# Kernel optimization log

Hardware: AMD Instinct MI355X
Metric: run time of the kernel (lower is better)

Reference implementation:

```python
import jax, jax.numpy as jnp
import numpy as np

EMBED_DIM = 1024
HEAD_DIM = 64


def setup_inputs() -> dict:
    key = jax.random.key(0)
    ks = jax.random.split(key, 7)
    s_in = EMBED_DIM ** -0.5  # torch Linear default init scale
    x = jax.random.normal(ks[0], (4, 4096, EMBED_DIM), dtype=jnp.float32)
    Wk = jax.random.uniform(ks[1], (HEAD_DIM, EMBED_DIM), jnp.float32, -s_in, s_in)
    bk = jax.random.uniform(ks[2], (HEAD_DIM,), jnp.float32, -s_in, s_in)
    Wq = jax.random.uniform(ks[3], (HEAD_DIM, EMBED_DIM), jnp.float32, -s_in, s_in)
    bq = jax.random.uniform(ks[4], (HEAD_DIM,), jnp.float32, -s_in, s_in)
    Wv = jax.random.uniform(ks[5], (HEAD_DIM, EMBED_DIM), jnp.float32, -s_in, s_in)
    bv = jax.random.uniform(ks[6], (HEAD_DIM,), jnp.float32, -s_in, s_in)
    return {"x": x, "Wq": Wq, "bq": bq, "Wk": Wk, "bk": bk, "Wv": Wv, "bv": bv}


def reference(x, Wq, bq, Wk, bk, Wv, bv):
    # torch Linear: y = x @ W.T + b
    q = jnp.einsum('btc,dc->btd', x, Wq) + bq  # [B,T,D]
    k = jnp.einsum('btc,dc->btd', x, Wk) + bk
    v = jnp.einsum('btc,dc->btd', x, Wv) + bv
    scale = HEAD_DIM ** -0.5
    # NOTE: original divides by scale (multiplies by sqrt(head_dim)) -- faithful
    scores = jnp.einsum('btd,bsd->bts', q, k) / scale  # [B,T,T]
    attn_weights = jax.nn.softmax(scores, axis=-1)
    return jnp.einsum('bts,bsd->btd', attn_weights, v)
```

## Files before the change

### kernel.cpp

```cpp
#include <hip/hip_runtime.h>

#define BATCH 4
#define SEQ   4096
#define CDIM  1024
#define DDIM  64
#define NROW  (BATCH * SEQ)
#define NSPL  8
#define SEG   (NROW * DDIM)

typedef _Float16 f16;
typedef _Float16 f16x8 __attribute__((ext_vector_type(8)));
typedef _Float16 f16x4 __attribute__((ext_vector_type(4)));
typedef __fp16   h16x2 __attribute__((ext_vector_type(2)));
typedef float    f32x4 __attribute__((ext_vector_type(4)));

#define MFMA32(a, b, c) __builtin_amdgcn_mfma_f32_16x16x32_f16((a), (b), (c), 0, 0, 0)
#define MFMA16(a, b, c) __builtin_amdgcn_mfma_f32_16x16x16f16((a), (b), (c), 0, 0, 0)

#define GLDS(g, l)                                                            \
  __builtin_amdgcn_global_load_lds((const __attribute__((address_space(1))) void*)(g), \
                                   (__attribute__((address_space(3))) void*)(l), 16, 0, 0)

#define QSCALE 11.5415603f

__device__ inline f16x8 cvt8(f32x4 a, f32x4 b) {
  h16x2 p0 = __builtin_amdgcn_cvt_pkrtz(a[0], a[1]);
  h16x2 p1 = __builtin_amdgcn_cvt_pkrtz(a[2], a[3]);
  h16x2 p2 = __builtin_amdgcn_cvt_pkrtz(b[0], b[1]);
  h16x2 p3 = __builtin_amdgcn_cvt_pkrtz(b[2], b[3]);
  f16x8 r;
  r[0] = p0[0]; r[1] = p0[1]; r[2] = p1[0]; r[3] = p1[1];
  r[4] = p2[0]; r[5] = p2[1]; r[6] = p3[0]; r[7] = p3[1];
  return r;
}

__device__ inline f16x4 cvt4(float a, float b, float c, float d) {
  h16x2 lo = __builtin_amdgcn_cvt_pkrtz(a, b);
  h16x2 hi = __builtin_amdgcn_cvt_pkrtz(c, d);
  f16x4 r;
  r[0] = lo[0]; r[1] = lo[1]; r[2] = hi[0]; r[3] = hi[1];
  return r;
}

__global__ __launch_bounds__(256) void prep_w_kernel(const float* __restrict__ Wq,
                                                     const float* __restrict__ Wk,
                                                     const float* __restrict__ Wv,
                                                     f16* __restrict__ wf2) {
  const int t = blockIdx.x * 256 + threadIdx.x;
  const int lane = t & 63;
  const int s = t >> 6;
  const int mt = s % 12, ck = s / 12;
  const int mat = mt >> 2, tile = mt & 3;
  const int n = lane & 15, quad = lane >> 4;
  const float* W = (mat == 0) ? Wq : (mat == 1) ? Wk : Wv;
  const float* src = W + (size_t)(tile * 16 + n) * CDIM + ck * 32 + quad * 8;
  const f32x4 a = *(const f32x4*)src;
  const f32x4 b = *(const f32x4*)(src + 4);
  *(f16x8*)(wf2 + (size_t)t * 8) = cvt8(a, b);
}

__global__ __launch_bounds__(512, 4) void proj_kernel(const float* __restrict__ x,
                                                      const f16* __restrict__ wf2,
                                                      const float* __restrict__ bq,
                                                      const float* __restrict__ bk,
                                                      const float* __restrict__ bv,
                                                      f16* __restrict__ qs,
                                                      f16* __restrict__ ks,
                                                      f16* __restrict__ vc) {
  __shared__ __attribute__((aligned(16))) char smem[2][16384];
  const int tid = threadIdx.x, lane = tid & 63, w = tid >> 6;
  const int n = lane & 15, quad = lane >> 4;
  const int rowbase = blockIdx.x * 32;

  const float* xsrc[2] = {nullptr, nullptr};
  const f16* wsrc[2] = {nullptr, nullptr};
  int xdst[2] = {0, 0}, wdst[2] = {0, 0};
  if (w < 2) {
#pragma unroll
    for (int j = 0; j < 2; ++j) {
      const int i = 2 * w + j;
      xsrc[j] = x + (size_t)(rowbase + i * 8 + (lane >> 3)) * CDIM +
                (((lane & 7) ^ ((lane >> 3) & 7)) * 4);
      xdst[j] = i * 1024;
    }
  } else {
#pragma unroll
    for (int j = 0; j < 2; ++j) {
      const int mt = 2 * (w - 2) + j;
      wsrc[j] = wf2 + (size_t)mt * 512 + lane * 8;
      wdst[j] = 4096 + mt * 1024;
    }
  }

  auto issue = [&](int ck, int b) {
    char* base = &smem[b][0];
    if (w < 2) {
#pragma unroll
      for (int j = 0; j < 2; ++j) GLDS(xsrc[j] + ck * 32, base + xdst[j]);
    } else {
#pragma unroll
      for (int j = 0; j < 2; ++j) GLDS(wsrc[j] + (size_t)ck * 6144, base + wdst[j]);
    }
  };

  const int rt = w >> 2, mtb = 3 * (w & 3);
  f32x4 acc[3];
#pragma unroll
  for (int i = 0; i < 3; ++i) acc[i] = (f32x4){0.f, 0.f, 0.f, 0.f};

  issue(0, 0);
  for (int ck = 0; ck < 32; ++ck) {
    const int b = ck & 1;
    __syncthreads();
    if (ck + 1 < 32) issue(ck + 1, b ^ 1);
    const char* base = &smem[b][0];
    const char* xb = base + (rt * 16 + n) * 128;
    const f32x4 xa = *(const f32x4*)(xb + ((((quad << 1) ^ (n & 7)) << 4)));
    const f32x4 xc = *(const f32x4*)(xb + (((((quad << 1) | 1) ^ (n & 7)) << 4)));
    const f16x8 a = cvt8(xa, xc);
#pragma unroll
    for (int i2 = 0; i2 < 3; ++i2) {
      const f16x8 bf = *(const f16x8*)(base + 4096 + (mtb + i2) * 1024 + lane * 16);
      acc[i2] = MFMA32(a, bf, acc[i2]);
    }
  }

  const int r0 = rowbase + rt * 16 + quad * 4;
#pragma unroll
  for (int i2 = 0; i2 < 3; ++i2) {
    const int mt = mtb + i2;
    const int mat = mt >> 2, tile = mt & 3;
    const int d = tile * 16 + n;
    const f32x4 aa = acc[i2];
    if (mat == 0) {
      const float bi = bq[d];
#pragma unroll
      for (int r = 0; r < 4; ++r)
        qs[(size_t)(r0 + r) * DDIM + d] = (f16)((aa[r] + bi) * QSCALE);
    } else if (mat == 1) {
      const float bi = bk[d];
#pragma unroll
      for (int r = 0; r < 4; ++r) {
        const int t = r0 + r;
        const int col = ((((d >> 3) ^ (t & 7)) << 3) | (d & 7));
        ks[(size_t)t * DDIM + col] = (f16)(aa[r] + bi);
      }
    } else {
      const float bi = bv[d];
      const int bb = r0 >> 12;
      const int tl = r0 & (SEQ - 1);
      const int ck2 = tl >> 6;
      const int bsw = (((tl & 63) >> 2) ^ n) << 2;
      *(f16x4*)(vc + ((size_t)(bb * 64 + ck2) * 64 + d) * 64 + bsw) =
          cvt4(aa[0] + bi, aa[1] + bi, aa[2] + bi, aa[3] + bi);
    }
  }
}

template <int NSPLIT>
__global__ __launch_bounds__(256, 4) void attn_kernel(const f16* __restrict__ qs,
                                                      const f16* __restrict__ ks,
                                                      const f16* __restrict__ vc,
                                                      float* __restrict__ outp,
                                                      f16* __restrict__ pacc,
                                                      float* __restrict__ pm,
                                                      float* __restrict__ pl) {
  __shared__ __attribute__((aligned(16))) f16 lk[2][4096];
  __shared__ __attribute__((aligned(16))) f16 lv[2][4096];
  const int tid = threadIdx.x, lane = tid & 63, w = tid >> 6;
  const int n = lane & 15, quad = lane >> 4;
  const int split = blockIdx.x % NSPLIT;
  const int rowblk = blockIdx.x / NSPLIT;
  const int row0 = rowblk * 128 + w * 32;
  const int bb = row0 >> 12;
  const int kbase = split * (SEQ / NSPLIT);
  const int kc0 = kbase >> 6;
  const int NC = SEQ / NSPLIT / 64;

  const f16* ksb = ks + (size_t)bb * SEQ * DDIM;
  const f16* vcb = vc + (size_t)bb * 64 * 4096;

  auto issue = [&](int c, int buf) {
#pragma unroll
    for (int i = 0; i < 2; ++i) {
      const int id = 2 * w + i;
      GLDS(ksb + (size_t)(kbase + c * 64) * 64 + id * 512 + lane * 8, &lk[buf][id * 512]);
      GLDS(vcb + (size_t)(kc0 + c) * 4096 + id * 512 + lane * 8, &lv[buf][id * 512]);
    }
  };

  f16x8 qf[2][2];
#pragma unroll
  for (int g = 0; g < 2; ++g)
#pragma unroll
    for (int hh = 0; hh < 2; ++hh)
      qf[g][hh] = *(const f16x8*)(qs + (size_t)(row0 + g * 16 + n) * DDIM + hh * 32 + quad * 8);

  const int kswz = (quad ^ (n & 7)) << 3;
  int vswz[4];
#pragma unroll
  for (int st = 0; st < 4; ++st) vswz[st] = ((((st << 2) | quad) ^ n) << 2);

  f32x4 acc[2][4];
  float m[2] = {-1e30f, -1e30f}, ll[2] = {0.f, 0.f};
#pragma unroll
  for (int g = 0; g < 2; ++g)
#pragma unroll
    for (int t = 0; t < 4; ++t) acc[g][t] = (f32x4){0.f, 0.f, 0.f, 0.f};

  issue(0, 0);
  for (int c = 0; c < NC; ++c) {
    const int b = c & 1;
    __syncthreads();
    if (c + 1 < NC) issue(c + 1, b ^ 1);

    f32x4 s[2][4];
#pragma unroll
    for (int st = 0; st < 4; ++st) {
      const f16* lkr = &lk[b][(st * 16 + n) * 64];
      const f16x8 klo = *(const f16x8*)(lkr + kswz);
      const f16x8 khi = *(const f16x8*)(lkr + (kswz ^ 32));
#pragma unroll
      for (int g = 0; g < 2; ++g) {
        f32x4 z = (f32x4){0.f, 0.f, 0.f, 0.f};
        z = MFMA32(klo, qf[g][0], z);
        s[g][st] = MFMA32(khi, qf[g][1], z);
      }
    }

    f16x4 pq[2][4];
#pragma unroll
    for (int g = 0; g < 2; ++g) {
      f32x4 mx;
#pragma unroll
      for (int r = 0; r < 4; ++r)
        mx[r] = fmaxf(fmaxf(s[g][0][r], s[g][1][r]), fmaxf(s[g][2][r], s[g][3][r]));
      float mloc = fmaxf(fmaxf(mx[0], mx[1]), fmaxf(mx[2], mx[3]));
      mloc = fmaxf(mloc, __shfl_xor(mloc, 16));
      mloc = fmaxf(mloc, __shfl_xor(mloc, 32));
      const float mnew = fmaxf(m[g], mloc);
      const float alpha = __builtin_amdgcn_exp2f(m[g] - mnew);
      m[g] = mnew;
      float psum = 0.f;
#pragma unroll
      for (int st = 0; st < 4; ++st) {
        f32x4 p;
#pragma unroll
        for (int r = 0; r < 4; ++r) p[r] = __builtin_amdgcn_exp2f(s[g][st][r] - mnew);
        psum += (p[0] + p[1]) + (p[2] + p[3]);
        pq[g][st] = cvt4(p[0], p[1], p[2], p[3]);
      }
      ll[g] = ll[g] * alpha + psum;
#pragma unroll
      for (int t = 0; t < 4; ++t) acc[g][t] *= alpha;
    }

#pragma unroll
    for (int dt = 0; dt < 4; ++dt) {
      const f16* lvr = &lv[b][(dt * 16 + n) * 64];
#pragma unroll
      for (int st = 0; st < 4; ++st) {
        const f16x4 va = *(const f16x4*)(lvr + vswz[st]);
        acc[0][dt] = MFMA16(va, pq[0][st], acc[0][dt]);
        acc[1][dt] = MFMA16(va, pq[1][st], acc[1][dt]);
      }
    }
  }

  float lred[2];
#pragma unroll
  for (int g = 0; g < 2; ++g) {
    float l = ll[g];
    l += __shfl_xor(l, 16);
    l += __shfl_xor(l, 32);
    lred[g] = l;
  }

  if (NSPLIT == 1) {
#pragma unroll
    for (int g = 0; g < 2; ++g) {
      const float inv = 1.0f / lred[g];
      const int q = row0 + g * 16 + n;
#pragma unroll
      for (int t = 0; t < 4; ++t) {
        f32x4 o = acc[g][t];
#pragma unroll
        for (int r = 0; r < 4; ++r) o[r] *= inv;
        *(f32x4*)(outp + (size_t)q * DDIM + t * 16 + quad * 4) = o;
      }
    }
  } else {
#pragma unroll
    for (int g = 0; g < 2; ++g) {
      const int q = row0 + g * 16 + n;
#pragma unroll
      for (int t = 0; t < 4; ++t)
        *(f16x4*)(pacc + ((size_t)split * NROW + q) * DDIM + t * 16 + quad * 4) =
            cvt4(acc[g][t][0], acc[g][t][1], acc[g][t][2], acc[g][t][3]);
      if (quad == 0) {
        pm[split * NROW + q] = m[g];
        pl[split * NROW + q] = lred[g];
      }
    }
  }
}

template <int NSPLIT>
__global__ __launch_bounds__(256) void combine_kernel(const f16* __restrict__ pacc,
                                                      const float* __restrict__ pm,
                                                      const float* __restrict__ pl,
                                                      float* __restrict__ out) {
  const int idx = blockIdx.x * 256 + threadIdx.x;
  const int row = idx >> 4;
  const int c = (idx & 15) * 4;
  float mm = pm[row];
#pragma unroll
  for (int s = 1; s < NSPLIT; ++s) mm = fmaxf(mm, pm[s * NROW + row]);
  float L = 0.f;
  f32x4 o = (f32x4){0.f, 0.f, 0.f, 0.f};
#pragma unroll
  for (int s = 0; s < NSPLIT; ++s) {
    const float e = __builtin_amdgcn_exp2f(pm[s * NROW + row] - mm);
    L += pl[s * NROW + row] * e;
    const f16x4 a = *(const f16x4*)(pacc + ((size_t)s * NROW + row) * DDIM + c);
#pragma unroll
    for (int j = 0; j < 4; ++j) o[j] += (float)a[j] * e;
  }
  const float inv = 1.0f / L;
#pragma unroll
  for (int j = 0; j < 4; ++j) o[j] *= inv;
  *(f32x4*)(out + (size_t)row * DDIM + c) = o;
}

extern "C" void kernel_launch(void* const* d_in, const int* in_sizes, int n_in,
                              void* d_out, int out_size, void* d_ws, size_t ws_size,
                              hipStream_t stream) {
  const float* x  = (const float*)d_in[0];
  const float* Wq = (const float*)d_in[1];
  const float* bq = (const float*)d_in[2];
  const float* Wk = (const float*)d_in[3];
  const float* bk = (const float*)d_in[4];
  const float* Wv = (const float*)d_in[5];
  const float* bv = (const float*)d_in[6];
  float* out = (float*)d_out;

  f16* wf2 = (f16*)d_ws;
  f16* qs = wf2 + 3 * 65536;
  f16* ks = qs + (size_t)SEG;
  f16* vc = ks + (size_t)SEG;
  f16* pacc = vc + (size_t)SEG;
  float* pm = (float*)(pacc + (size_t)NSPL * SEG);
  float* pl = pm + (size_t)NSPL * NROW;
  const size_t need = (size_t)((char*)(pl + (size_t)NSPL * NROW) - (char*)d_ws);

  prep_w_kernel<<<dim3(96), dim3(256), 0, stream>>>(Wq, Wk, Wv, wf2);
  proj_kernel<<<dim3(512), dim3(512), 0, stream>>>(x, wf2, bq, bk, bv, qs, ks, vc);

  if (ws_size >= need) {
    attn_kernel<NSPL><<<dim3(128 * NSPL), dim3(256), 0, stream>>>(qs, ks, vc, nullptr, pacc, pm, pl);
    combine_kernel<NSPL><<<dim3(NROW * 16 / 256), dim3(256), 0, stream>>>(pacc, pm, pl, out);
  } else {
    attn_kernel<1><<<dim3(128), dim3(256), 0, stream>>>(qs, ks, vc, out, nullptr, nullptr, nullptr);
  }
}
```

Baseline: 186.9 us.

## Replace LDS-staged projection with direct register loads and double-buffered prefetch

The projection kernel no longer stages x and weights through shared memory with global_load_lds and per-chunk barriers. Each of 4 waves now loads its x rows and weight fragments straight into registers, with a two-deep software prefetch, and computes 2 row tiles × 3 output tiles. Block size drops from 512 to 256 threads. This removes the LDS round trip and the barriers, at the cost of more registers per thread and redundant global loads of x across waves, which now rely on the cache.

```diff
diff --git a/kernel.cpp b/kernel.cpp
--- a/kernel.cpp
+++ b/kernel.cpp
@@ -59,100 +59,94 @@
   *(f16x8*)(wf2 + (size_t)t * 8) = cvt8(a, b);
 }
 
-__global__ __launch_bounds__(512, 4) void proj_kernel(const float* __restrict__ x,
-                                                      const f16* __restrict__ wf2,
-                                                      const float* __restrict__ bq,
-                                                      const float* __restrict__ bk,
-                                                      const float* __restrict__ bv,
-                                                      f16* __restrict__ qs,
-                                                      f16* __restrict__ ks,
-                                                      f16* __restrict__ vc) {
-  __shared__ __attribute__((aligned(16))) char smem[2][16384];
+__global__ __launch_bounds__(256) void proj_kernel(const float* __restrict__ x,
+                                                   const f16* __restrict__ wf2,
+                                                   const float* __restrict__ bq,
+                                                   const float* __restrict__ bk,
+                                                   const float* __restrict__ bv,
+                                                   f16* __restrict__ qs,
+                                                   f16* __restrict__ ks,
+                                                   f16* __restrict__ vc) {
   const int tid = threadIdx.x, lane = tid & 63, w = tid >> 6;
   const int n = lane & 15, quad = lane >> 4;
   const int rowbase = blockIdx.x * 32;
-
-  const float* xsrc[2] = {nullptr, nullptr};
-  const f16* wsrc[2] = {nullptr, nullptr};
-  int xdst[2] = {0, 0}, wdst[2] = {0, 0};
-  if (w < 2) {
-#pragma unroll
-    for (int j = 0; j < 2; ++j) {
-      const int i = 2 * w + j;
-      xsrc[j] = x + (size_t)(rowbase + i * 8 + (lane >> 3)) * CDIM +
-                (((lane & 7) ^ ((lane >> 3) & 7)) * 4);
-      xdst[j] = i * 1024;
-    }
-  } else {
-#pragma unroll
-    for (int j = 0; j < 2; ++j) {
-      const int mt = 2 * (w - 2) + j;
-      wsrc[j] = wf2 + (size_t)mt * 512 + lane * 8;
-      wdst[j] = 4096 + mt * 1024;
-    }
-  }
-
-  auto issue = [&](int ck, int b) {
-    char* base = &smem[b][0];
-    if (w < 2) {
-#pragma unroll
-      for (int j = 0; j < 2; ++j) GLDS(xsrc[j] + ck * 32, base + xdst[j]);
-    } else {
-#pragma unroll
-      for (int j = 0; j < 2; ++j) GLDS(wsrc[j] + (size_t)ck * 6144, base + wdst[j]);
-    }
-  };
-
-  const int rt = w >> 2, mtb = 3 * (w & 3);
-  f32x4 acc[3];
-#pragma unroll
-  for (int i = 0; i < 3; ++i) acc[i] = (f32x4){0.f, 0.f, 0.f, 0.f};
-
-  issue(0, 0);
-  for (int ck = 0; ck < 32; ++ck) {
-    const int b = ck & 1;
-    __syncthreads();
-    if (ck + 1 < 32) issue(ck + 1, b ^ 1);
-    const char* base = &smem[b][0];
-    const char* xb = base + (rt * 16 + n) * 128;
-    const f32x4 xa = *(const f32x4*)(xb + ((((quad << 1) ^ (n & 7)) << 4)));
-    const f32x4 xc = *(const f32x4*)(xb + (((((quad << 1) | 1) ^ (n & 7)) << 4)));
-    const f16x8 a = cvt8(xa, xc);
+  const int mtb = 3 * w;
+
+  const float* xp0 = x + (size_t)(rowbase + n) * CDIM + quad * 8;
+  const float* xp1 = x + (size_t)(rowbase + 16 + n) * CDIM + quad * 8;
+  const f16* wp = wf2 + (size_t)mtb * 512 + lane * 8;
+
+  f32x4 acc[6];
+#pragma unroll
+  for (int i = 0; i < 6; ++i) acc[i] = (f32x4){0.f, 0.f, 0.f, 0.f};
+
+#define LOADCK(ck, A0, C0, A1, C1, W0, W1, W2)                  \
+  do {                                                          \
+    const float* xq0 = xp0 + (ck) * 32;                         \
+    const float* xq1 = xp1 + (ck) * 32;                         \
+    A0 = *(const f32x4*)xq0; C0 = *(const f32x4*)(xq0 + 4);     \
+    A1 = *(const f32x4*)xq1; C1 = *(const f32x4*)(xq1 + 4);     \
+    const f16* wq = wp + (size_t)(ck) * 6144;                   \
+    W0 = *(const f16x8*)(wq);                                   \
+    W1 = *(const f16x8*)(wq + 512);                             \
+    W2 = *(const f16x8*)(wq + 1024);                            \
+  } while (0)
+
+#define COMPCK(A0, C0, A1, C1, W0, W1, W2)                      \
+  do {                                                          \
+    const f16x8 fa0 = cvt8(A0, C0);                             \
+    const f16x8 fa1 = cvt8(A1, C1);                             \
+    acc[0] = MFMA32(fa0, W0, acc[0]);                           \
+    acc[3] = MFMA32(fa1, W0, acc[3]);                           \
+    acc[1] = MFMA32(fa0, W1, acc[1]);                           \
+    acc[4] = MFMA32(fa1, W1, acc[4]);                           \
+    acc[2] = MFMA32(fa0, W2, acc[2]);                           \
+    acc[5] = MFMA32(fa1, W2, acc[5]);                           \
+  } while (0)
+
+  f32x4 a0, c0, a1, c1, b0, d0, b1, d1;
+  f16x8 u0, u1, u2, v0, v1, v2;
+  LOADCK(0, a0, c0, a1, c1, u0, u1, u2);
+  for (int ck = 0; ck < 32; ck += 2) {
+    LOADCK(ck + 1, b0, d0, b1, d1, v0, v1, v2);
+    COMPCK(a0, c0, a1, c1, u0, u1, u2);
+    if (ck + 2 < 32) LOADCK(ck + 2, a0, c0, a1, c1, u0, u1, u2);
+    COMPCK(b0, d0, b1, d1, v0, v1, v2);
+  }
+#undef LOADCK
+#undef COMPCK
+
+#pragma unroll
+  for (int t = 0; t < 2; ++t) {
+    const int r0 = rowbase + t * 16 + quad * 4;
 #pragma unroll
     for (int i2 = 0; i2 < 3; ++i2) {
-      const f16x8 bf = *(const f16x8*)(base + 4096 + (mtb + i2) * 1024 + lane * 16);
-      acc[i2] = MFMA32(a, bf, acc[i2]);
-    }
-  }
-
-  const int r0 = rowbase + rt * 16 + quad * 4;
-#pragma unroll
-  for (int i2 = 0; i2 < 3; ++i2) {
-    const int mt = mtb + i2;
-    const int mat = mt >> 2, tile = mt & 3;
-    const int d = tile * 16 + n;
-    const f32x4 aa = acc[i2];
-    if (mat == 0) {
-      const float bi = bq[d];
-#pragma unroll
-      for (int r = 0; r < 4; ++r)
-        qs[(size_t)(r0 + r) * DDIM + d] = (f16)((aa[r] + bi) * QSCALE);
-    } else if (mat == 1) {
-      const float bi = bk[d];
-#pragma unroll
-      for (int r = 0; r < 4; ++r) {
-        const int t = r0 + r;
-        const int col = ((((d >> 3) ^ (t & 7)) << 3) | (d & 7));
-        ks[(size_t)t * DDIM + col] = (f16)(aa[r] + bi);
-      }
-    } else {
-      const float bi = bv[d];
-      const int bb = r0 >> 12;
-      const int tl = r0 & (SEQ - 1);
-      const int ck2 = tl >> 6;
-      const int bsw = (((tl & 63) >> 2) ^ n) << 2;
-      *(f16x4*)(vc + ((size_t)(bb * 64 + ck2) * 64 + d) * 64 + bsw) =
-          cvt4(aa[0] + bi, aa[1] + bi, aa[2] + bi, aa[3] + bi);
+      const int mt = mtb + i2;
+      const int mat = mt >> 2, tile = mt & 3;
+      const int d = tile * 16 + n;
+      const f32x4 aa = acc[t * 3 + i2];
+      if (mat == 0) {
+        const float bi = bq[d];
+#pragma unroll
+        for (int r = 0; r < 4; ++r)
+          qs[(size_t)(r0 + r) * DDIM + d] = (f16)((aa[r] + bi) * QSCALE);
+      } else if (mat == 1) {
+        const float bi = bk[d];
+#pragma unroll
+        for (int r = 0; r < 4; ++r) {
+          const int tt = r0 + r;
+          const int col = ((((d >> 3) ^ (tt & 7)) << 3) | (d & 7));
+          ks[(size_t)tt * DDIM + col] = (f16)(aa[r] + bi);
+        }
+      } else {
+        const float bi = bv[d];
+        const int bb = r0 >> 12;
+        const int tl = r0 & (SEQ - 1);
+        const int ck2 = tl >> 6;
+        const int bsw = (((tl & 63) >> 2) ^ n) << 2;
+        *(f16x4*)(vc + ((size_t)(bb * 64 + ck2) * 64 + d) * 64 + bsw) =
+            cvt4(aa[0] + bi, aa[1] + bi, aa[2] + bi, aa[3] + bi);
+      }
     }
   }
 }
@@ -354,7 +348,7 @@
   const size_t need = (size_t)((char*)(pl + (size_t)NSPL * NROW) - (char*)d_ws);
 
   prep_w_kernel<<<dim3(96), dim3(256), 0, stream>>>(Wq, Wk, Wv, wf2);
-  proj_kernel<<<dim3(512), dim3(512), 0, stream>>>(x, wf2, bq, bk, bv, qs, ks, vc);
+  proj_kernel<<<dim3(512), dim3(256), 0, stream>>>(x, wf2, bq, bk, bv, qs, ks, vc);
 
   if (ws_size >= need) {
     attn_kernel<NSPL><<<dim3(128 * NSPL), dim3(256), 0, stream>>>(qs, ks, vc, nullptr, pacc, pm, pl);
```

Measured after the change: 171.7 us. 8.1% less time.
